# Kernel optimization log

Measured on AMD Instinct MI355X. Metric: run time of the kernel, lower is better.

## Reference

```python
import jax, jax.numpy as jnp
import numpy as np

B, L, D, H = 2, 2048, 1024, 16
HD = D // H


def _xavier(key, out_f, in_f):
    std = (2.0 / (in_f + out_f)) ** 0.5
    return jax.random.normal(key, (out_f, in_f), dtype=jnp.float32) * std


def setup_inputs() -> dict:
    key = jax.random.key(0)
    k = jax.random.split(key, 8)
    Q = jax.random.normal(k[0], (B, L, D), dtype=jnp.float32)
    K = jax.random.normal(k[1], (B, L, D), dtype=jnp.float32)
    V = jax.random.normal(k[2], (B, L, D), dtype=jnp.float32)
    mask = jnp.tril(jnp.ones((L, L), dtype=jnp.int32))[None, None]  # causal [1,1,L,L]
    wq = _xavier(k[3], D, D)
    wk = _xavier(k[4], D, D)
    wv = _xavier(k[5], D, D)
    wo = _xavier(k[6], D, D)
    bo = jnp.zeros((D,), dtype=jnp.float32)
    return {"Q": Q, "K": K, "V": V, "mask": mask,
            "wq": wq, "wk": wk, "wv": wv, "wo": wo, "bo": bo}


def reference(Q, K, V, mask, wq, wk, wv, wo, bo):
    N, Lq, Dm = Q.shape
    # projections: X @ W^T (Linear stores [out, in])
    q = (Q @ wq.T).reshape(N, Lq, H, HD).transpose(0, 2, 1, 3)  # [N,H,L,hd]
    kk = (K @ wk.T).reshape(N, Lq, H, HD).transpose(0, 2, 1, 3)
    v = (V @ wv.T).reshape(N, Lq, H, HD).transpose(0, 2, 1, 3)
    score = jnp.einsum('bhqd,bhkd->bhqk', q, kk) / jnp.sqrt(jnp.float32(HD))
    score = jnp.where(mask == 0, -jnp.inf, score)
    weights = jax.nn.softmax(score, axis=-1)
    attn = jnp.einsum('bhqk,bhkd->bhqd', weights, v)
    out = attn.transpose(0, 2, 1, 3).reshape(N, Lq, Dm)
    return out @ wo.T + bo
```

## Files before the change

### kernel.cpp

```cpp
#include <hip/hip_runtime.h>
#include <hip/hip_bf16.h>


#define B_ 2
#define L_ 2048
#define D_ 1024
#define H_ 16
#define HD_ 64
#define NA_ ((size_t)B_ * L_ * D_)
#define NW_ ((size_t)D_ * D_)

typedef __attribute__((ext_vector_type(8))) short bf16x8;
typedef __attribute__((ext_vector_type(4))) float f32x4;
typedef __hip_bfloat16 bf16;

__device__ __forceinline__ void async_load16(const void* g, void* l) {
  __builtin_amdgcn_global_load_lds((const __attribute__((address_space(1))) void*)g,
                                   (__attribute__((address_space(3))) void*)l,
                                   16, 0, 0);
}

__global__ __launch_bounds__(256) void xcvt_kernel(const float* __restrict__ q,
                                                   const float* __restrict__ k,
                                                   const float* __restrict__ v,
                                                   const float* __restrict__ w0,
                                                   const float* __restrict__ w1,
                                                   const float* __restrict__ w2,
                                                   const float* __restrict__ w3,
                                                   bf16* __restrict__ dst) {
  const int y = blockIdx.y;
  size_t i = ((size_t)blockIdx.x * 256 + threadIdx.x) * 4;
  const float* src;
  size_t soff = i;
  if (y < 3) {
    src = (y == 0) ? q : (y == 1) ? k : v;
  } else {
    int w = (int)(i >> 20);
    src = (w == 0) ? w0 : (w == 1) ? w1 : (w == 2) ? w2 : w3;
    soff = i & (NW_ - 1);
  }
  float4 vv = *(const float4*)(src + soff);
  union { bf16 h[4]; uint2 u; } pk;
  pk.h[0] = __float2bfloat16(vv.x);
  pk.h[1] = __float2bfloat16(vv.y);
  pk.h[2] = __float2bfloat16(vv.z);
  pk.h[3] = __float2bfloat16(vv.w);
  *(uint2*)(dst + (size_t)y * NA_ + i) = pk.u;
}

#define TS_ 136
__global__ __launch_bounds__(256) void gemm_qkv(const bf16* __restrict__ Qb,
                                                const bf16* __restrict__ Kb,
                                                const bf16* __restrict__ Vb,
                                                const bf16* __restrict__ Wb,
                                                bf16* __restrict__ qp,
                                                bf16* __restrict__ kp,
                                                bf16* __restrict__ vtp) {
  __shared__ __align__(16) bf16 smem[128 * TS_];
  bf16* As = smem;
  bf16* Bs = smem + 128 * 32;
  const int tid = threadIdx.x;
  const int wv = tid >> 6, lane = tid & 63;
  const int quad = lane >> 4, l16 = lane & 15;
  const int wm = wv & 1, wn = wv >> 1;
  const int m0 = blockIdx.x * 128, n0 = blockIdx.y * 128;
  const int z = blockIdx.z;
  const bf16* X = (z == 0) ? Qb : (z == 1) ? Kb : Vb;
  const bf16* W = Wb + (size_t)z * NW_;

  f32x4 acc[4][4];
#pragma unroll
  for (int i = 0; i < 4; i++)
#pragma unroll
    for (int j = 0; j < 4; j++) acc[i][j] = (f32x4){0.f, 0.f, 0.f, 0.f};

  for (int k0 = 0; k0 < D_; k0 += 32) {
#pragma unroll
    for (int it = 0; it < 2; it++) {
      int c = (wv * 2 + it) * 64 + lane;
      int row = c >> 2, cc = c & 3;
      async_load16(X + (size_t)(m0 + row) * D_ + k0 + cc * 8, (char*)As + c * 16);
      async_load16(W + (size_t)(n0 + row) * D_ + k0 + cc * 8, (char*)Bs + c * 16);
    }
    __syncthreads();
    bf16x8 af[4], bfr[4];
#pragma unroll
    for (int mi = 0; mi < 4; mi++)
      af[mi] = *(const bf16x8*)&As[(wm * 64 + mi * 16 + l16) * 32 + quad * 8];
#pragma unroll
    for (int ni = 0; ni < 4; ni++)
      bfr[ni] = *(const bf16x8*)&Bs[(wn * 64 + ni * 16 + l16) * 32 + quad * 8];
#pragma unroll
    for (int mi = 0; mi < 4; mi++)
#pragma unroll
      for (int ni = 0; ni < 4; ni++)
        acc[mi][ni] = __builtin_amdgcn_mfma_f32_16x16x32_bf16(af[mi], bfr[ni],
                                                              acc[mi][ni], 0, 0, 0);
    __syncthreads();
  }

  if (z == 2) {
    bf16* T = smem;
#pragma unroll
    for (int mi = 0; mi < 4; mi++) {
#pragma unroll
      for (int ni = 0; ni < 4; ni++) {
        int n_loc = wn * 64 + ni * 16 + l16;
        int m_loc = wm * 64 + mi * 16 + quad * 4;
        union { bf16 hx[4]; uint2 d; } pk;
#pragma unroll
        for (int r = 0; r < 4; r++) pk.hx[r] = __float2bfloat16(acc[mi][ni][r]);
        *(uint2*)&T[n_loc * TS_ + m_loc] = pk.d;
      }
    }
    __syncthreads();
#pragma unroll
    for (int p = 0; p < 8; p++) {
      int n_loc = p * 16 + (tid >> 4);
      int m_loc = (tid & 15) * 8;
      bf16x8 vv = *(const bf16x8*)&T[n_loc * TS_ + m_loc];
      int n = n0 + n_loc;
      int m = m0 + m_loc;
      int bb = m >> 11, l = m & (L_ - 1);
      int hh = n >> 6, hd = n & 63;
      *(bf16x8*)&vtp[((size_t)((bb * H_ + hh) * HD_ + hd)) * L_ + l] = vv;
    }
  } else {
    const float sc = (z == 0) ? 0.125f : 1.0f;
    bf16* dst = (z == 0) ? qp : kp;
#pragma unroll
    for (int mi = 0; mi < 4; mi++) {
#pragma unroll
      for (int ni = 0; ni < 4; ni++) {
        int n = n0 + wn * 64 + ni * 16 + l16;
#pragma unroll
        for (int r = 0; r < 4; r++) {
          int m = m0 + wm * 64 + mi * 16 + quad * 4 + r;
          dst[(size_t)m * D_ + n] = __float2bfloat16(acc[mi][ni][r] * sc);
        }
      }
    }
  }
}

__global__ __launch_bounds__(256) void attn_kernel(const bf16* __restrict__ qp,
                                                   const bf16* __restrict__ kp,
                                                   const bf16* __restrict__ vt,
                                                   bf16* __restrict__ attn) {
  __shared__ __align__(16) bf16 Kt[2][64 * 64];
  __shared__ __align__(16) bf16 Vt[2][64 * 64];
  __shared__ __align__(16) bf16 P[4][16 * 72];
  const int tid = threadIdx.x;
  const int wv = tid >> 6, lane = tid & 63;
  const int quad = lane >> 4, l16 = lane & 15;
  const int h = blockIdx.x, band = 31 - (int)blockIdx.y, b = blockIdx.z;

  const int rq = band * 64 + wv * 16 + l16;
  bf16x8 qa[2];
#pragma unroll
  for (int kk = 0; kk < 2; kk++)
    qa[kk] = *(const bf16x8*)&qp[((size_t)(b * L_ + rq)) * D_ + h * HD_ +
                                 kk * 32 + quad * 8];

  f32x4 O[4];
#pragma unroll
  for (int t = 0; t < 4; t++) O[t] = (f32x4){0.f, 0.f, 0.f, 0.f};
  float l = 0.f;

  const int csw = quad ^ (l16 & 7);

  auto stage = [&](int j, int buf) {
    const int j0 = j * 64;
#pragma unroll
    for (int it = 0; it < 2; it++) {
      int slot = (wv * 2 + it) * 64 + lane;
      int row = slot >> 3, c = (slot & 7) ^ (row & 7);
      async_load16(kp + ((size_t)(b * L_ + j0 + row)) * D_ + h * HD_ + c * 8,
                   (char*)Kt[buf] + slot * 16);
      async_load16(vt + ((size_t)((b * H_ + h) * HD_ + row)) * L_ + j0 + c * 8,
                   (char*)Vt[buf] + slot * 16);
    }
  };

  stage(0, 0);
  for (int j = 0; j <= band; j++) {
    const int buf = j & 1;
    const int j0 = j * 64;
    __syncthreads();
    if (j < band) stage(j + 1, buf ^ 1);

    f32x4 s[4];
#pragma unroll
    for (int ss = 0; ss < 4; ss++) {
      int krow = ss * 16 + l16;
      bf16x8 kb0 = *(const bf16x8*)&Kt[buf][krow * 64 + csw * 8];
      bf16x8 kb1 = *(const bf16x8*)&Kt[buf][krow * 64 + (csw ^ 4) * 8];
      f32x4 t = (f32x4){0.f, 0.f, 0.f, 0.f};
      t = __builtin_amdgcn_mfma_f32_16x16x32_bf16(kb0, qa[0], t, 0, 0, 0);
      t = __builtin_amdgcn_mfma_f32_16x16x32_bf16(kb1, qa[1], t, 0, 0, 0);
      s[ss] = t;
    }

    if (j == band) {
#pragma unroll
      for (int ss = 0; ss < 4; ss++)
#pragma unroll
        for (int r = 0; r < 4; r++) {
          int key = j0 + ss * 16 + quad * 4 + r;
          if (key > rq) s[ss][r] = -1e30f;
        }
    }

#pragma unroll
    for (int ss = 0; ss < 4; ss++) {
      float p0 = __expf(s[ss][0]), p1 = __expf(s[ss][1]);
      float p2 = __expf(s[ss][2]), p3 = __expf(s[ss][3]);
      l += (p0 + p1) + (p2 + p3);
      union { bf16 hx[4]; uint2 d; } pk;
      pk.hx[0] = __float2bfloat16(p0);
      pk.hx[1] = __float2bfloat16(p1);
      pk.hx[2] = __float2bfloat16(p2);
      pk.hx[3] = __float2bfloat16(p3);
      *(uint2*)&P[wv][l16 * 72 + ss * 16 + quad * 4] = pk.d;
    }

    asm volatile("s_waitcnt lgkmcnt(0)" ::: "memory");

#pragma unroll
    for (int kk = 0; kk < 2; kk++) {
      bf16x8 pa = *(const bf16x8*)&P[wv][l16 * 72 + kk * 32 + quad * 8];
#pragma unroll
      for (int t = 0; t < 4; t++) {
        bf16x8 vb = *(const bf16x8*)&Vt[buf][(t * 16 + l16) * 64 + (csw ^ (kk * 4)) * 8];
        O[t] = __builtin_amdgcn_mfma_f32_16x16x32_bf16(pa, vb, O[t], 0, 0, 0);
      }
    }
  }

  l += __shfl_xor(l, 16, 64);
  l += __shfl_xor(l, 32, 64);
  float lq[4];
#pragma unroll
  for (int r = 0; r < 4; r++) lq[r] = __shfl(l, quad * 4 + r, 64);

#pragma unroll
  for (int t = 0; t < 4; t++) {
#pragma unroll
    for (int r = 0; r < 4; r++) {
      int row = band * 64 + wv * 16 + quad * 4 + r;
      attn[((size_t)(b * L_ + row)) * D_ + h * HD_ + t * 16 + l16] =
          __float2bfloat16(O[t][r] / lq[r]);
    }
  }
}

__global__ __launch_bounds__(256) void gemm_out(const bf16* __restrict__ X,
                                                const bf16* __restrict__ W,
                                                const float* __restrict__ bias,
                                                float* __restrict__ out) {
  __shared__ __align__(16) bf16 As[64 * 32];
  __shared__ __align__(16) bf16 Bs[128 * 32];
  const int tid = threadIdx.x;
  const int wv = tid >> 6, lane = tid & 63;
  const int quad = lane >> 4, l16 = lane & 15;
  const int wm = wv & 1, wn = wv >> 1;
  const int m0 = blockIdx.x * 64, n0 = blockIdx.y * 128;

  f32x4 acc[2][4];
#pragma unroll
  for (int i = 0; i < 2; i++)
#pragma unroll
    for (int j = 0; j < 4; j++) acc[i][j] = (f32x4){0.f, 0.f, 0.f, 0.f};

  for (int k0 = 0; k0 < D_; k0 += 32) {
    {
      int c = tid;
      int row = c >> 2, cc = c & 3;
      async_load16(X + (size_t)(m0 + row) * D_ + k0 + cc * 8, (char*)As + c * 16);
    }
#pragma unroll
    for (int it = 0; it < 2; it++) {
      int c = (wv * 2 + it) * 64 + lane;
      int row = c >> 2, cc = c & 3;
      async_load16(W + (size_t)(n0 + row) * D_ + k0 + cc * 8, (char*)Bs + c * 16);
    }
    __syncthreads();
    bf16x8 af[2], bfr[4];
#pragma unroll
    for (int mi = 0; mi < 2; mi++)
      af[mi] = *(const bf16x8*)&As[(wm * 32 + mi * 16 + l16) * 32 + quad * 8];
#pragma unroll
    for (int ni = 0; ni < 4; ni++)
      bfr[ni] = *(const bf16x8*)&Bs[(wn * 64 + ni * 16 + l16) * 32 + quad * 8];
#pragma unroll
    for (int mi = 0; mi < 2; mi++)
#pragma unroll
      for (int ni = 0; ni < 4; ni++)
        acc[mi][ni] = __builtin_amdgcn_mfma_f32_16x16x32_bf16(af[mi], bfr[ni],
                                                              acc[mi][ni], 0, 0, 0);
    __syncthreads();
  }

#pragma unroll
  for (int mi = 0; mi < 2; mi++) {
#pragma unroll
    for (int ni = 0; ni < 4; ni++) {
      int n = n0 + wn * 64 + ni * 16 + l16;
      float bval = bias[n];
#pragma unroll
      for (int r = 0; r < 4; r++) {
        int m = m0 + wm * 32 + mi * 16 + quad * 4 + r;
        out[(size_t)m * D_ + n] = acc[mi][ni][r] + bval;
      }
    }
  }
}

extern "C" void kernel_launch(void* const* d_in, const int* in_sizes, int n_in,
                              void* d_out, int out_size, void* d_ws, size_t ws_size,
                              hipStream_t stream) {
  const float* Q  = (const float*)d_in[0];
  const float* K  = (const float*)d_in[1];
  const float* V  = (const float*)d_in[2];
  const float* wq = (const float*)d_in[4];
  const float* wk = (const float*)d_in[5];
  const float* wvp = (const float*)d_in[6];
  const float* wo = (const float*)d_in[7];
  const float* bo = (const float*)d_in[8];
  float* out = (float*)d_out;

  bf16* base = (bf16*)d_ws;
  bf16* Qb = base;
  bf16* Kb = Qb + NA_;
  bf16* Vb = Kb + NA_;
  bf16* Wb = Vb + NA_;
  bf16* qp = Wb + 4 * NW_;
  bf16* kp = qp + NA_;
  bf16* vt = kp + NA_;
  bf16* at = vt + NA_;

  xcvt_kernel<<<dim3(NA_ / 1024, 4), 256, 0, stream>>>(Q, K, V, wq, wk, wvp, wo, base);
  gemm_qkv<<<dim3(32, 8, 3), 256, 0, stream>>>(Qb, Kb, Vb, Wb, qp, kp, vt);
  attn_kernel<<<dim3(H_, L_ / 64, B_), 256, 0, stream>>>(qp, kp, vt, at);
  gemm_out<<<dim3(64, 8), 256, 0, stream>>>(at, Wb + 3 * NW_, bo, out);
}
```

Measured before the change: 218.7 us.

## Process 128-row query tiles per attention block and swizzle GEMM block order for XCDs

```diff
diff --git a/kernel.cpp b/kernel.cpp
--- a/kernel.cpp
+++ b/kernel.cpp
@@ -63,8 +63,10 @@
   const int wv = tid >> 6, lane = tid & 63;
   const int quad = lane >> 4, l16 = lane & 15;
   const int wm = wv & 1, wn = wv >> 1;
-  const int m0 = blockIdx.x * 128, n0 = blockIdx.y * 128;
-  const int z = blockIdx.z;
+  const int id = blockIdx.x + 32 * blockIdx.y + 256 * blockIdx.z;
+  const int swz = (id & 7) * 96 + (id >> 3);
+  const int m0 = (swz & 31) * 128, n0 = ((swz >> 5) & 7) * 128;
+  const int z = swz >> 8;
   const bf16* X = (z == 0) ? Qb : (z == 1) ? Kb : Vb;
   const bf16* W = Wb + (size_t)z * NW_;
 
@@ -149,25 +151,36 @@
                                                    bf16* __restrict__ attn) {
   __shared__ __align__(16) bf16 Kt[2][64 * 64];
   __shared__ __align__(16) bf16 Vt[2][64 * 64];
-  __shared__ __align__(16) bf16 P[4][16 * 72];
+  __shared__ __align__(16) bf16 P0[4][16 * 72];
+  __shared__ __align__(16) bf16 P1[4][16 * 72];
   const int tid = threadIdx.x;
   const int wv = tid >> 6, lane = tid & 63;
   const int quad = lane >> 4, l16 = lane & 15;
-  const int h = blockIdx.x, band = 31 - (int)blockIdx.y, b = blockIdx.z;
-
-  const int rq = band * 64 + wv * 16 + l16;
-  bf16x8 qa[2];
-#pragma unroll
-  for (int kk = 0; kk < 2; kk++)
-    qa[kk] = *(const bf16x8*)&qp[((size_t)(b * L_ + rq)) * D_ + h * HD_ +
-                                 kk * 32 + quad * 8];
-
-  f32x4 O[4];
-#pragma unroll
-  for (int t = 0; t < 4; t++) O[t] = (f32x4){0.f, 0.f, 0.f, 0.f};
-  float l = 0.f;
+  const int h = blockIdx.x, bi = 15 - (int)blockIdx.y, b = blockIdx.z;
+  const int r0 = bi * 128;
+
+  const int rq0 = r0 + wv * 32 + l16;
+  const int rq1 = rq0 + 16;
+  bf16x8 qa0[2], qa1[2];
+#pragma unroll
+  for (int kk = 0; kk < 2; kk++) {
+    qa0[kk] = *(const bf16x8*)&qp[((size_t)(b * L_ + rq0)) * D_ + h * HD_ +
+                                  kk * 32 + quad * 8];
+    qa1[kk] = *(const bf16x8*)&qp[((size_t)(b * L_ + rq1)) * D_ + h * HD_ +
+                                  kk * 32 + quad * 8];
+  }
+
+  f32x4 O0[4], O1[4];
+#pragma unroll
+  for (int t = 0; t < 4; t++) {
+    O0[t] = (f32x4){0.f, 0.f, 0.f, 0.f};
+    O1[t] = (f32x4){0.f, 0.f, 0.f, 0.f};
+  }
+  float l0 = 0.f, l1 = 0.f;
 
   const int csw = quad ^ (l16 & 7);
+  const int dt = 2 * bi + (wv >> 1);
+  const int jmax = 2 * bi + 1;
 
   auto stage = [&](int j, int buf) {
     const int j0 = j * 64;
@@ -183,73 +196,98 @@
   };
 
   stage(0, 0);
-  for (int j = 0; j <= band; j++) {
+  for (int j = 0; j <= jmax; j++) {
     const int buf = j & 1;
     const int j0 = j * 64;
     __syncthreads();
-    if (j < band) stage(j + 1, buf ^ 1);
-
-    f32x4 s[4];
+    if (j < jmax) stage(j + 1, buf ^ 1);
+    if (j > dt) continue;
+
+    f32x4 s0[4], s1[4];
 #pragma unroll
     for (int ss = 0; ss < 4; ss++) {
       int krow = ss * 16 + l16;
       bf16x8 kb0 = *(const bf16x8*)&Kt[buf][krow * 64 + csw * 8];
       bf16x8 kb1 = *(const bf16x8*)&Kt[buf][krow * 64 + (csw ^ 4) * 8];
       f32x4 t = (f32x4){0.f, 0.f, 0.f, 0.f};
-      t = __builtin_amdgcn_mfma_f32_16x16x32_bf16(kb0, qa[0], t, 0, 0, 0);
-      t = __builtin_amdgcn_mfma_f32_16x16x32_bf16(kb1, qa[1], t, 0, 0, 0);
-      s[ss] = t;
-    }
-
-    if (j == band) {
+      t = __builtin_amdgcn_mfma_f32_16x16x32_bf16(kb0, qa0[0], t, 0, 0, 0);
+      t = __builtin_amdgcn_mfma_f32_16x16x32_bf16(kb1, qa0[1], t, 0, 0, 0);
+      s0[ss] = t;
+      f32x4 u = (f32x4){0.f, 0.f, 0.f, 0.f};
+      u = __builtin_amdgcn_mfma_f32_16x16x32_bf16(kb0, qa1[0], u, 0, 0, 0);
+      u = __builtin_amdgcn_mfma_f32_16x16x32_bf16(kb1, qa1[1], u, 0, 0, 0);
+      s1[ss] = u;
+    }
+
+    if (j == dt) {
 #pragma unroll
       for (int ss = 0; ss < 4; ss++)
 #pragma unroll
         for (int r = 0; r < 4; r++) {
           int key = j0 + ss * 16 + quad * 4 + r;
-          if (key > rq) s[ss][r] = -1e30f;
+          if (key > rq0) s0[ss][r] = -1e30f;
+          if (key > rq1) s1[ss][r] = -1e30f;
         }
     }
 
 #pragma unroll
     for (int ss = 0; ss < 4; ss++) {
-      float p0 = __expf(s[ss][0]), p1 = __expf(s[ss][1]);
-      float p2 = __expf(s[ss][2]), p3 = __expf(s[ss][3]);
-      l += (p0 + p1) + (p2 + p3);
+      float p0 = __expf(s0[ss][0]), p1 = __expf(s0[ss][1]);
+      float p2 = __expf(s0[ss][2]), p3 = __expf(s0[ss][3]);
+      l0 += (p0 + p1) + (p2 + p3);
       union { bf16 hx[4]; uint2 d; } pk;
       pk.hx[0] = __float2bfloat16(p0);
       pk.hx[1] = __float2bfloat16(p1);
       pk.hx[2] = __float2bfloat16(p2);
       pk.hx[3] = __float2bfloat16(p3);
-      *(uint2*)&P[wv][l16 * 72 + ss * 16 + quad * 4] = pk.d;
+      *(uint2*)&P0[wv][l16 * 72 + ss * 16 + quad * 4] = pk.d;
+      float q0 = __expf(s1[ss][0]), q1 = __expf(s1[ss][1]);
+      float q2 = __expf(s1[ss][2]), q3 = __expf(s1[ss][3]);
+      l1 += (q0 + q1) + (q2 + q3);
+      union { bf16 hx[4]; uint2 d; } qk;
+      qk.hx[0] = __float2bfloat16(q0);
+      qk.hx[1] = __float2bfloat16(q1);
+      qk.hx[2] = __float2bfloat16(q2);
+      qk.hx[3] = __float2bfloat16(q3);
+      *(uint2*)&P1[wv][l16 * 72 + ss * 16 + quad * 4] = qk.d;
     }
 
     asm volatile("s_waitcnt lgkmcnt(0)" ::: "memory");
 
 #pragma unroll
     for (int kk = 0; kk < 2; kk++) {
-      bf16x8 pa = *(const bf16x8*)&P[wv][l16 * 72 + kk * 32 + quad * 8];
+      bf16x8 pa0 = *(const bf16x8*)&P0[wv][l16 * 72 + kk * 32 + quad * 8];
+      bf16x8 pa1 = *(const bf16x8*)&P1[wv][l16 * 72 + kk * 32 + quad * 8];
 #pragma unroll
       for (int t = 0; t < 4; t++) {
         bf16x8 vb = *(const bf16x8*)&Vt[buf][(t * 16 + l16) * 64 + (csw ^ (kk * 4)) * 8];
-        O[t] = __builtin_amdgcn_mfma_f32_16x16x32_bf16(pa, vb, O[t], 0, 0, 0);
+        O0[t] = __builtin_amdgcn_mfma_f32_16x16x32_bf16(pa0, vb, O0[t], 0, 0, 0);
+        O1[t] = __builtin_amdgcn_mfma_f32_16x16x32_bf16(pa1, vb, O1[t], 0, 0, 0);
       }
     }
   }
 
-  l += __shfl_xor(l, 16, 64);
-  l += __shfl_xor(l, 32, 64);
-  float lq[4];
-#pragma unroll
-  for (int r = 0; r < 4; r++) lq[r] = __shfl(l, quad * 4 + r, 64);
+  l0 += __shfl_xor(l0, 16, 64);
+  l0 += __shfl_xor(l0, 32, 64);
+  l1 += __shfl_xor(l1, 16, 64);
+  l1 += __shfl_xor(l1, 32, 64);
+  float lq0[4], lq1[4];
+#pragma unroll
+  for (int r = 0; r < 4; r++) {
+    lq0[r] = __shfl(l0, quad * 4 + r, 64);
+    lq1[r] = __shfl(l1, quad * 4 + r, 64);
+  }
 
 #pragma unroll
   for (int t = 0; t < 4; t++) {
 #pragma unroll
     for (int r = 0; r < 4; r++) {
-      int row = band * 64 + wv * 16 + quad * 4 + r;
-      attn[((size_t)(b * L_ + row)) * D_ + h * HD_ + t * 16 + l16] =
-          __float2bfloat16(O[t][r] / lq[r]);
+      int row0 = r0 + wv * 32 + quad * 4 + r;
+      int row1 = row0 + 16;
+      attn[((size_t)(b * L_ + row0)) * D_ + h * HD_ + t * 16 + l16] =
+          __float2bfloat16(O0[t][r] / lq0[r]);
+      attn[((size_t)(b * L_ + row1)) * D_ + h * HD_ + t * 16 + l16] =
+          __float2bfloat16(O1[t][r] / lq1[r]);
     }
   }
 }
@@ -264,7 +302,9 @@
   const int wv = tid >> 6, lane = tid & 63;
   const int quad = lane >> 4, l16 = lane & 15;
   const int wm = wv & 1, wn = wv >> 1;
-  const int m0 = blockIdx.x * 64, n0 = blockIdx.y * 128;
+  const int id = blockIdx.x + 64 * blockIdx.y;
+  const int swz = (id & 7) * 64 + (id >> 3);
+  const int m0 = (swz & 63) * 64, n0 = (swz >> 6) * 128;
 
   f32x4 acc[2][4];
 #pragma unroll
@@ -341,6 +381,6 @@
 
   xcvt_kernel<<<dim3(NA_ / 1024, 4), 256, 0, stream>>>(Q, K, V, wq, wk, wvp, wo, base);
   gemm_qkv<<<dim3(32, 8, 3), 256, 0, stream>>>(Qb, Kb, Vb, Wb, qp, kp, vt);
-  attn_kernel<<<dim3(H_, L_ / 64, B_), 256, 0, stream>>>(qp, kp, vt, at);
+  attn_kernel<<<dim3(H_, 16, B_), 256, 0, stream>>>(qp, kp, vt, at);
   gemm_out<<<dim3(64, 8), 256, 0, stream>>>(at, Wb + 3 * NW_, bo, out);
 }
```

After: 233.3 us. 6.7% more time.
